# Performance work log

Hardware: AMD Instinct MI355X
Metric: run time of the kernel (lower is better)

Reference implementation:

```python
import jax, jax.numpy as jnp
import numpy as np

B, C, IN, OUT = 256, 919, 400, 100

def setup_inputs() -> dict:
    key = jax.random.key(0)
    k1, k2 = jax.random.split(key)
    inputs = jax.random.normal(k1, (B, C, IN), dtype=jnp.float32)
    # glorot-style scaling for kernel
    kernel = jax.random.normal(k2, (1, C, IN, OUT), dtype=jnp.float32) * (1.0 / np.sqrt(IN))
    bias = jnp.zeros((1, C, OUT), dtype=jnp.float32)
    return {"inputs": inputs, "kernel": kernel, "bias": bias}

def reference(inputs, kernel, bias):
    # Original: broadcast (B,C,IN,1) * (1,C,IN,OUT), reduce over IN, add bias.
    # Equivalent fused form: per-category batched GEMM.
    # inputs: (B, C, IN); kernel: (1, C, IN, OUT) -> out: (B, C, OUT)
    out = jnp.einsum('bci,cio->bco', inputs, kernel[0])
    out = out + bias  # (1, C, OUT) broadcasts over batch
    return out  # activation is None (linear)
```

## Files before the change

kernel.cpp:

```cpp
#include <hip/hip_runtime.h>
#include <stdint.h>

#define NCAT  919
#define KDIM  400
#define NDIM  100
#define BK    32
#define NSTEP 13
#define KPAD  408
#define NROWS 100

typedef float  f32x4  __attribute__((ext_vector_type(4)));
typedef __bf16 bf16x8 __attribute__((ext_vector_type(8)));
typedef __bf16 bf16x2 __attribute__((ext_vector_type(2)));

__global__ void __launch_bounds__(512, 2)
cat_dense(const float* __restrict__ in, const float* __restrict__ wt,
          const float* __restrict__ bias, float* __restrict__ out)
{
  __shared__ __bf16 wlds[NROWS * KPAD];

  const int ob   = blockIdx.x;
  const int xcd  = ob & 7;
  const int bidx = ob >> 3;
  const int c    = (xcd < 7 ? xcd * 115 : 805 + (xcd - 7) * 114) + bidx;

  const int tid  = threadIdx.x;
  const int lane = tid & 63;
  const int wave = tid >> 6;
  const int rl   = lane & 15;
  const int kg   = (lane >> 4) * 8;

  const size_t rstride = (size_t)NCAT * KDIM;
  const float* gA0 = in + (size_t)c * KDIM + (size_t)(wave * 32 + rl) * rstride;
  const float* gA1 = gA0 + (size_t)16 * rstride;
  const float* gW  = wt + (size_t)c * (KDIM * NDIM);

  f32x4 areg[4][2][2];

#define LOADA(T) do {                                                      \
    const int kb_ = (T) * BK + kg;                                         \
    const int s_  = (T) & 3;                                               \
    if (kb_ + 8 <= KDIM) {     \
      areg[s_][0][0] = *(const f32x4*)(gA0 + kb_);                         \
      areg[s_][0][1] = *(const f32x4*)(gA0 + kb_ + 4);                     \
      areg[s_][1][0] = *(const f32x4*)(gA1 + kb_);                         \
      areg[s_][1][1] = *(const f32x4*)(gA1 + kb_ + 4);                     \
    } else {                                                               \
      areg[s_][0][0] = f32x4{0,0,0,0}; areg[s_][0][1] = f32x4{0,0,0,0};    \
      areg[s_][1][0] = f32x4{0,0,0,0}; areg[s_][1][1] = f32x4{0,0,0,0};    \
    }                                                                      \
  } while (0)

  LOADA(0);
  LOADA(1);

  #pragma unroll
  for (int i = 0; i < 10; ++i) {
    const int pc = tid + i * 512;
    if (pc < 5000) {
      const int kp = pc / 25;
      const int nq = pc - kp * 25;
      const int k  = kp * 2;
      const float* p = gW + (size_t)k * NDIM + nq * 4;
      const f32x4 w0 = *(const f32x4*)p;
      const f32x4 w1 = *(const f32x4*)(p + NDIM);
      #pragma unroll
      for (int j = 0; j < 4; ++j) {
        bf16x2 pk = { (__bf16)w0[j], (__bf16)w1[j] };
        *(bf16x2*)&wlds[(nq * 4 + j) * KPAD + k] = pk;
      }
    }
  }
  __syncthreads();

  f32x4 acc[2][7];
  #pragma unroll
  for (int m = 0; m < 2; ++m)
    #pragma unroll
    for (int n = 0; n < 7; ++n) acc[m][n] = f32x4{0, 0, 0, 0};

  #pragma unroll
  for (int t = 0; t < NSTEP; ++t) {
    const int pp = t & 3;
    bf16x8 a0, a1;
    #pragma unroll
    for (int j = 0; j < 4; ++j) {
      a0[j]     = (__bf16)areg[pp][0][0][j];
      a0[4 + j] = (__bf16)areg[pp][0][1][j];
      a1[j]     = (__bf16)areg[pp][1][0][j];
      a1[4 + j] = (__bf16)areg[pp][1][1][j];
    }
    if ((t & 1) == 0 && t + 2 < NSTEP) {
      LOADA(t + 2);
      if (t + 3 < NSTEP) LOADA(t + 3);
    }
    const int kb2  = t * BK + kg;
    const int koff = (kb2 <= KDIM - 8) ? kb2 : (KDIM - 8);
    #pragma unroll
    for (int n = 0; n < 7; ++n) {
      const int brow = n * 16 + (n == 6 ? (rl & 3) : rl);
      bf16x8 b = *(const bf16x8*)&wlds[brow * KPAD + koff];
      acc[0][n] = __builtin_amdgcn_mfma_f32_16x16x32_bf16(a0, b, acc[0][n], 0, 0, 0);
      acc[1][n] = __builtin_amdgcn_mfma_f32_16x16x32_bf16(a1, b, acc[1][n], 0, 0, 0);
    }
  }

  const float* gB = bias + (size_t)c * NDIM;
  float* gO = out + (size_t)c * NDIM;
  #pragma unroll
  for (int n = 0; n < 7; ++n) {
    const int col = n * 16 + rl;
    if (col < NDIM) {
      const float bv = gB[col];
      #pragma unroll
      for (int m = 0; m < 2; ++m) {
        const int r0 = wave * 32 + m * 16 + (lane >> 4) * 4;
        #pragma unroll
        for (int j = 0; j < 4; ++j) {
          gO[(size_t)(r0 + j) * ((size_t)NCAT * NDIM) + col] = acc[m][n][j] + bv;
        }
      }
    }
  }
}

extern "C" void kernel_launch(void* const* d_in, const int* in_sizes, int n_in,
                              void* d_out, int out_size, void* d_ws, size_t ws_size,
                              hipStream_t stream) {
  const float* in   = (const float*)d_in[0];
  const float* wt   = (const float*)d_in[1];
  const float* bias = (const float*)d_in[2];
  float* o          = (float*)d_out;
  cat_dense<<<dim3(NCAT), dim3(512), 0, stream>>>(in, wt, bias, o);
}
```

Baseline: 148.3 us.

## Split weight staging into two halves and overlap second half with MFMA loop

The weight tile is now staged into LDS in two phases. Rows k<224 are loaded and converted before the main loop. The loads for the remaining k are issued early and written to LDS at step 6, behind a mid-loop barrier. The A-register prefetch ring grows from 4 to 6 stages with a deeper, hand-scheduled load pattern. The goal is to hide weight load latency behind compute and start MFMAs sooner, at the cost of more registers (risking occupancy at 2 blocks/CU) and an extra __syncthreads.

```diff
diff --git a/kernel.cpp b/kernel.cpp
--- a/kernel.cpp
+++ b/kernel.cpp
@@ -35,43 +35,65 @@
   const float* gA1 = gA0 + (size_t)16 * rstride;
   const float* gW  = wt + (size_t)c * (KDIM * NDIM);
 
-  f32x4 areg[4][2][2];
+  f32x4 areg[6][2][2];
 
 #define LOADA(T) do {                                                      \
     const int kb_ = (T) * BK + kg;                                         \
-    const int s_  = (T) & 3;                                               \
     if (kb_ + 8 <= KDIM) {     \
-      areg[s_][0][0] = *(const f32x4*)(gA0 + kb_);                         \
-      areg[s_][0][1] = *(const f32x4*)(gA0 + kb_ + 4);                     \
-      areg[s_][1][0] = *(const f32x4*)(gA1 + kb_);                         \
-      areg[s_][1][1] = *(const f32x4*)(gA1 + kb_ + 4);                     \
+      areg[(T) % 6][0][0] = *(const f32x4*)(gA0 + kb_);                    \
+      areg[(T) % 6][0][1] = *(const f32x4*)(gA0 + kb_ + 4);                \
+      areg[(T) % 6][1][0] = *(const f32x4*)(gA1 + kb_);                    \
+      areg[(T) % 6][1][1] = *(const f32x4*)(gA1 + kb_ + 4);                \
     } else {                                                               \
-      areg[s_][0][0] = f32x4{0,0,0,0}; areg[s_][0][1] = f32x4{0,0,0,0};    \
-      areg[s_][1][0] = f32x4{0,0,0,0}; areg[s_][1][1] = f32x4{0,0,0,0};    \
+      areg[(T) % 6][0][0] = f32x4{0,0,0,0};                                \
+      areg[(T) % 6][0][1] = f32x4{0,0,0,0};                                \
+      areg[(T) % 6][1][0] = f32x4{0,0,0,0};                                \
+      areg[(T) % 6][1][1] = f32x4{0,0,0,0};                                \
     }                                                                      \
   } while (0)
 
-  LOADA(0);
-  LOADA(1);
+  LOADA(0); LOADA(1); LOADA(2); LOADA(3);
 
+  f32x4 wa0[6], wa1[6];
   #pragma unroll
-  for (int i = 0; i < 10; ++i) {
+  for (int i = 0; i < 6; ++i) {
     const int pc = tid + i * 512;
-    if (pc < 5000) {
-      const int kp = pc / 25;
-      const int nq = pc - kp * 25;
-      const int k  = kp * 2;
-      const float* p = gW + (size_t)k * NDIM + nq * 4;
-      const f32x4 w0 = *(const f32x4*)p;
-      const f32x4 w1 = *(const f32x4*)(p + NDIM);
+    if (pc < 2800) {
+      const int nq = pc / 112;
+      const int kp = pc - nq * 112;
+      const float* p = gW + (size_t)(2 * kp) * NDIM + nq * 4;
+      wa0[i] = *(const f32x4*)p;
+      wa1[i] = *(const f32x4*)(p + NDIM);
+    }
+  }
+  #pragma unroll
+  for (int i = 0; i < 6; ++i) {
+    const int pc = tid + i * 512;
+    if (pc < 2800) {
+      const int nq = pc / 112;
+      const int kp = pc - nq * 112;
       #pragma unroll
       for (int j = 0; j < 4; ++j) {
-        bf16x2 pk = { (__bf16)w0[j], (__bf16)w1[j] };
-        *(bf16x2*)&wlds[(nq * 4 + j) * KPAD + k] = pk;
+        bf16x2 pk = { (__bf16)wa0[i][j], (__bf16)wa1[i][j] };
+        *(bf16x2*)&wlds[(nq * 4 + j) * KPAD + 2 * kp] = pk;
       }
     }
   }
   __syncthreads();
+
+  f32x4 wb0[5], wb1[5];
+  #pragma unroll
+  for (int i = 0; i < 5; ++i) {
+    const int pc = tid + i * 512;
+    if (pc < 2200) {
+      const int nq = pc / 88;
+      const int kp = 112 + (pc - nq * 88);
+      const float* p = gW + (size_t)(2 * kp) * NDIM + nq * 4;
+      wb0[i] = *(const f32x4*)p;
+      wb1[i] = *(const f32x4*)(p + NDIM);
+    }
+  }
+  __builtin_amdgcn_sched_barrier(0);
 
   f32x4 acc[2][7];
   #pragma unroll
@@ -81,7 +103,7 @@
 
   #pragma unroll
   for (int t = 0; t < NSTEP; ++t) {
-    const int pp = t & 3;
+    const int pp = t % 6;
     bf16x8 a0, a1;
     #pragma unroll
     for (int j = 0; j < 4; ++j) {
@@ -90,10 +112,10 @@
       a1[j]     = (__bf16)areg[pp][1][0][j];
       a1[4 + j] = (__bf16)areg[pp][1][1][j];
     }
-    if ((t & 1) == 0 && t + 2 < NSTEP) {
-      LOADA(t + 2);
-      if (t + 3 < NSTEP) LOADA(t + 3);
-    }
+    if (t == 0 || t == 2 || t == 4) { LOADA(t + 4); LOADA(t + 5); }
+    if (t == 7)                     { LOADA(10);    LOADA(11);    }
+    if (t == 9)                     { LOADA(12);                  }
+
     const int kb2  = t * BK + kg;
     const int koff = (kb2 <= KDIM - 8) ? kb2 : (KDIM - 8);
     #pragma unroll
@@ -102,6 +124,23 @@
       bf16x8 b = *(const bf16x8*)&wlds[brow * KPAD + koff];
       acc[0][n] = __builtin_amdgcn_mfma_f32_16x16x32_bf16(a0, b, acc[0][n], 0, 0, 0);
       acc[1][n] = __builtin_amdgcn_mfma_f32_16x16x32_bf16(a1, b, acc[1][n], 0, 0, 0);
+    }
+
+    if (t == 6) {
+      #pragma unroll
+      for (int i = 0; i < 5; ++i) {
+        const int pc = tid + i * 512;
+        if (pc < 2200) {
+          const int nq = pc / 88;
+          const int kp = 112 + (pc - nq * 88);
+          #pragma unroll
+          for (int j = 0; j < 4; ++j) {
+            bf16x2 pk = { (__bf16)wb0[i][j], (__bf16)wb1[i][j] };
+            *(bf16x2*)&wlds[(nq * 4 + j) * KPAD + 2 * kp] = pk;
+          }
+        }
+      }
+      __syncthreads();
     }
   }
 
```

Measured after the change: 156.0 us. 1.05x slower.

## Halve block to 256 threads with 64 rows per wave for more B-fragment reuse

Applied to the files above, without the earlier changes.

Cuts the workgroup from 8 to 4 waves, so each wave now computes 64 batch rows (4 M-tiles) instead of 32. Each LDS B fragment is reused across four MFMAs instead of two. The A prefetch changes to a 3-stage ring with one load per step, and the weight staging loop is split to batch global loads before the conversion and LDS stores. In exchange, register pressure rises sharply (acc 4x7 plus 3x4x2 A registers), which risks spills or lower occupancy, and there are fewer waves to hide memory latency.

```diff
diff --git a/kernel.cpp b/kernel.cpp
--- a/kernel.cpp
+++ b/kernel.cpp
@@ -8,12 +8,13 @@
 #define NSTEP 13
 #define KPAD  408
 #define NROWS 100
+#define NTHR  256
 
 typedef float  f32x4  __attribute__((ext_vector_type(4)));
 typedef __bf16 bf16x8 __attribute__((ext_vector_type(8)));
 typedef __bf16 bf16x2 __attribute__((ext_vector_type(2)));
 
-__global__ void __launch_bounds__(512, 2)
+__global__ void __launch_bounds__(NTHR, 2)
 cat_dense(const float* __restrict__ in, const float* __restrict__ wt,
           const float* __restrict__ bias, float* __restrict__ out)
 {
@@ -31,77 +32,93 @@
   const int kg   = (lane >> 4) * 8;
 
   const size_t rstride = (size_t)NCAT * KDIM;
-  const float* gA0 = in + (size_t)c * KDIM + (size_t)(wave * 32 + rl) * rstride;
-  const float* gA1 = gA0 + (size_t)16 * rstride;
-  const float* gW  = wt + (size_t)c * (KDIM * NDIM);
+  const float* gA[4];
+  #pragma unroll
+  for (int mt = 0; mt < 4; ++mt)
+    gA[mt] = in + (size_t)c * KDIM + (size_t)(wave * 64 + mt * 16 + rl) * rstride;
+  const float* gW = wt + (size_t)c * (KDIM * NDIM);
 
-  f32x4 areg[4][2][2];
+  f32x4 areg[3][4][2];
 
 #define LOADA(T) do {                                                      \
     const int kb_ = (T) * BK + kg;                                         \
-    const int s_  = (T) & 3;                                               \
+    const int s_  = (T) % 3;                                               \
     if (kb_ + 8 <= KDIM) {     \
-      areg[s_][0][0] = *(const f32x4*)(gA0 + kb_);                         \
-      areg[s_][0][1] = *(const f32x4*)(gA0 + kb_ + 4);                     \
-      areg[s_][1][0] = *(const f32x4*)(gA1 + kb_);                         \
-      areg[s_][1][1] = *(const f32x4*)(gA1 + kb_ + 4);                     \
+      _Pragma("unroll")                                                    \
+      for (int mt_ = 0; mt_ < 4; ++mt_) {                                  \
+        areg[s_][mt_][0] = *(const f32x4*)(gA[mt_] + kb_);                 \
+        areg[s_][mt_][1] = *(const f32x4*)(gA[mt_] + kb_ + 4);             \
+      }                                                                    \
     } else {                                                               \
-      areg[s_][0][0] = f32x4{0,0,0,0}; areg[s_][0][1] = f32x4{0,0,0,0};    \
-      areg[s_][1][0] = f32x4{0,0,0,0}; areg[s_][1][1] = f32x4{0,0,0,0};    \
+      _Pragma("unroll")                                                    \
+      for (int mt_ = 0; mt_ < 4; ++mt_) {                                  \
+        areg[s_][mt_][0] = f32x4{0,0,0,0};                                 \
+        areg[s_][mt_][1] = f32x4{0,0,0,0};                                 \
+      }                                                                    \
     }                                                                      \
   } while (0)
 
-  LOADA(0);
-  LOADA(1);
+  LOADA(0); LOADA(1); LOADA(2);
 
   #pragma unroll
-  for (int i = 0; i < 10; ++i) {
-    const int pc = tid + i * 512;
-    if (pc < 5000) {
-      const int kp = pc / 25;
-      const int nq = pc - kp * 25;
-      const int k  = kp * 2;
-      const float* p = gW + (size_t)k * NDIM + nq * 4;
-      const f32x4 w0 = *(const f32x4*)p;
-      const f32x4 w1 = *(const f32x4*)(p + NDIM);
-      #pragma unroll
-      for (int j = 0; j < 4; ++j) {
-        bf16x2 pk = { (__bf16)w0[j], (__bf16)w1[j] };
-        *(bf16x2*)&wlds[(nq * 4 + j) * KPAD + k] = pk;
+  for (int g = 0; g < 4; ++g) {
+    f32x4 w0[5], w1[5];
+    #pragma unroll
+    for (int i = 0; i < 5; ++i) {
+      const int pc = tid + (g * 5 + i) * NTHR;
+      if (pc < 5000) {
+        const int kp = pc / 25;
+        const int nq = pc - kp * 25;
+        const float* p = gW + (size_t)(2 * kp) * NDIM + nq * 4;
+        w0[i] = *(const f32x4*)p;
+        w1[i] = *(const f32x4*)(p + NDIM);
+      }
+    }
+    #pragma unroll
+    for (int i = 0; i < 5; ++i) {
+      const int pc = tid + (g * 5 + i) * NTHR;
+      if (pc < 5000) {
+        const int kp = pc / 25;
+        const int nq = pc - kp * 25;
+        #pragma unroll
+        for (int j = 0; j < 4; ++j) {
+          bf16x2 pk = { (__bf16)w0[i][j], (__bf16)w1[i][j] };
+          *(bf16x2*)&wlds[(nq * 4 + j) * KPAD + 2 * kp] = pk;
+        }
       }
     }
   }
   __syncthreads();
 
-  f32x4 acc[2][7];
+  f32x4 acc[4][7];
   #pragma unroll
-  for (int m = 0; m < 2; ++m)
+  for (int m = 0; m < 4; ++m)
     #pragma unroll
     for (int n = 0; n < 7; ++n) acc[m][n] = f32x4{0, 0, 0, 0};
 
   #pragma unroll
   for (int t = 0; t < NSTEP; ++t) {
-    const int pp = t & 3;
-    bf16x8 a0, a1;
+    const int pp = t % 3;
+    bf16x8 a[4];
     #pragma unroll
-    for (int j = 0; j < 4; ++j) {
-      a0[j]     = (__bf16)areg[pp][0][0][j];
-      a0[4 + j] = (__bf16)areg[pp][0][1][j];
-      a1[j]     = (__bf16)areg[pp][1][0][j];
-      a1[4 + j] = (__bf16)areg[pp][1][1][j];
+    for (int mt = 0; mt < 4; ++mt) {
+      #pragma unroll
+      for (int j = 0; j < 4; ++j) {
+        a[mt][j]     = (__bf16)areg[pp][mt][0][j];
+        a[mt][4 + j] = (__bf16)areg[pp][mt][1][j];
+      }
     }
-    if ((t & 1) == 0 && t + 2 < NSTEP) {
-      LOADA(t + 2);
-      if (t + 3 < NSTEP) LOADA(t + 3);
-    }
+    if (t + 3 < NSTEP) LOADA(t + 3);
+
     const int kb2  = t * BK + kg;
     const int koff = (kb2 <= KDIM - 8) ? kb2 : (KDIM - 8);
     #pragma unroll
     for (int n = 0; n < 7; ++n) {
       const int brow = n * 16 + (n == 6 ? (rl & 3) : rl);
       bf16x8 b = *(const bf16x8*)&wlds[brow * KPAD + koff];
-      acc[0][n] = __builtin_amdgcn_mfma_f32_16x16x32_bf16(a0, b, acc[0][n], 0, 0, 0);
-      acc[1][n] = __builtin_amdgcn_mfma_f32_16x16x32_bf16(a1, b, acc[1][n], 0, 0, 0);
+      #pragma unroll
+      for (int mt = 0; mt < 4; ++mt)
+        acc[mt][n] = __builtin_amdgcn_mfma_f32_16x16x32_bf16(a[mt], b, acc[mt][n], 0, 0, 0);
     }
   }
 
@@ -113,11 +130,11 @@
     if (col < NDIM) {
       const float bv = gB[col];
       #pragma unroll
-      for (int m = 0; m < 2; ++m) {
-        const int r0 = wave * 32 + m * 16 + (lane >> 4) * 4;
+      for (int mt = 0; mt < 4; ++mt) {
+        const int r0 = wave * 64 + mt * 16 + (lane >> 4) * 4;
         #pragma unroll
         for (int j = 0; j < 4; ++j) {
-          gO[(size_t)(r0 + j) * ((size_t)NCAT * NDIM) + col] = acc[m][n][j] + bv;
+          gO[(size_t)(r0 + j) * ((size_t)NCAT * NDIM) + col] = acc[mt][n][j] + bv;
         }
       }
     }
@@ -131,5 +148,5 @@
   const float* wt   = (const float*)d_in[1];
   const float* bias = (const float*)d_in[2];
   float* o          = (float*)d_out;
-  cat_dense<<<dim3(NCAT), dim3(512), 0, stream>>>(in, wt, bias, o);
+  cat_dense<<<dim3(NCAT), dim3(NTHR), 0, stream>>>(in, wt, bias, o);
 }
```

New measurement: 181.5 us. 22.3% more time.
